# Kernel tuning notes

Hardware: AMD Instinct MI355X
Metric: run time of the kernel (lower is better)

## Reference

```python
import jax, jax.numpy as jnp
import numpy as np

GROUPS = 32
EPS = 1e-5
NHEAD = 8


def group_norm(x, gamma, beta):
    # x: [B, C, T]
    B, C, T = x.shape
    xg = x.reshape(B, GROUPS, C // GROUPS, T)
    mean = xg.mean(axis=(2, 3), keepdims=True)
    var = xg.var(axis=(2, 3), keepdims=True)
    xg = (xg - mean) * jax.lax.rsqrt(var + EPS)
    x = xg.reshape(B, C, T)
    return x * gamma[None, :, None] + beta[None, :, None]


def conv1x1(x, w, b):
    # x: [B, C_in, T], w: [C_out, C_in], b: [C_out]
    return jnp.einsum('oc,bct->bot', w, x) + b[None, :, None]


def setup_inputs() -> dict:
    key = jax.random.key(0)
    ks = jax.random.split(key, 4)
    B, C, T = 8, 512, 2048
    x = jax.random.normal(ks[0], (B, C, T), dtype=jnp.float32)
    w_qkv = jax.random.normal(ks[1], (3 * C, C), dtype=jnp.float32) * (1.0 / np.sqrt(C))
    b_qkv = jnp.zeros((3 * C,), dtype=jnp.float32)
    w_proj = jax.random.normal(ks[2], (C, C), dtype=jnp.float32) * (1.0 / np.sqrt(C))
    b_proj = jnp.zeros((C,), dtype=jnp.float32)
    return {
        'x': x,
        'gn1_gamma': jnp.ones((C,), jnp.float32), 'gn1_beta': jnp.zeros((C,), jnp.float32),
        'w_qkv': w_qkv, 'b_qkv': b_qkv,
        'gn2_gamma': jnp.ones((C,), jnp.float32), 'gn2_beta': jnp.zeros((C,), jnp.float32),
        'w_proj': w_proj, 'b_proj': b_proj,
    }


def qkv_attention(qkv):
    # qkv: [B, 3*H*ch, T] laid out as H blocks of (q ch, k ch, v ch)
    B, width, T = qkv.shape
    ch = width // (3 * NHEAD)
    qkv = qkv.reshape(B, NHEAD, 3 * ch, T)
    q, k, v = qkv[:, :, :ch], qkv[:, :, ch:2 * ch], qkv[:, :, 2 * ch:]
    scale = 1.0 / np.sqrt(np.sqrt(ch)).astype(np.float32)
    # scores: [B, H, T(q), T(k)]
    w = jnp.einsum('bhct,bhcs->bhts', q * scale, k * scale)
    w = jax.nn.softmax(w, axis=-1)  # max-subtract softmax, same math
    a = jnp.einsum('bhts,bhcs->bhct', w, v)
    return a.reshape(B, NHEAD * ch, T)


def reference(x, gn1_gamma, gn1_beta, w_qkv, b_qkv, gn2_gamma, gn2_beta, w_proj, b_proj):
    # x: [B, C, T]
    qkv = conv1x1(group_norm(x, gn1_gamma, gn1_beta), w_qkv, b_qkv)  # [B, 3C, T]
    h = qkv_attention(qkv)                                            # [B, C, T]
    h = conv1x1(group_norm(h, gn2_gamma, gn2_beta), w_proj, b_proj)   # [B, C, T]
    return x + h
```

## Files before the change

### kernel.cpp

```cpp
#include <hip/hip_runtime.h>

typedef unsigned short u16;
typedef unsigned int   u32;
typedef __attribute__((ext_vector_type(8))) short short8;
typedef __attribute__((ext_vector_type(4))) float floatx4;

__device__ inline u16 f2bf(float x) {
  union { float f; unsigned u; } v; v.f = x;
  unsigned r = v.u + 0x7FFFu + ((v.u >> 16) & 1u);
  return (u16)(r >> 16);
}
__device__ inline float bf2f(short s) {
  union { u32 u; float f; } v; v.u = ((u32)(u16)s) << 16; return v.f;
}
__device__ inline short8 ld8(const u16* p) {
  return *reinterpret_cast<const short8*>(p);
}
__device__ inline void async_ld16(const u16* g, u16* l) {
  unsigned loff = (unsigned)(unsigned long long)(void*)l;
  __builtin_amdgcn_global_load_lds(reinterpret_cast<const unsigned*>(g),
      reinterpret_cast<__attribute__((address_space(3))) unsigned*>(loff), 16, 0, 0);
}

__global__ __launch_bounds__(1024) void gncast(const float* __restrict__ x,
                                               const float* __restrict__ gamma,
                                               const float* __restrict__ beta,
                                               u16* __restrict__ xn,
                                               const float* __restrict__ wq,
                                               u16* __restrict__ wqb,
                                               const float* __restrict__ wp,
                                               u16* __restrict__ wpb) {
  __shared__ u16 tile[16 * 2048];
  float* stats = (float*)tile;
  const int tid = threadIdx.x;
  if (blockIdx.x >= 256) {
    int i = (blockIdx.x - 256) * 1024 + tid;
    const float* src; u16* dst; int j;
    if (i < 196608) { src = wq; dst = wqb; j = i; }
    else            { src = wp; dst = wpb; j = i - 196608; }
    float4 v = reinterpret_cast<const float4*>(src)[j];
    union { u16 u[4]; float2 f; } w;
    w.u[0] = f2bf(v.x); w.u[1] = f2bf(v.y); w.u[2] = f2bf(v.z); w.u[3] = f2bf(v.w);
    reinterpret_cast<float2*>(dst)[j] = w.f;
    return;
  }
  int b = blockIdx.x >> 5, g = blockIdx.x & 31;
  const float* base = x + ((long)b * 512 + g * 16) * 2048;
  float s = 0.f, ss = 0.f;
  for (int i = tid; i < 8192; i += 1024) {
    float4 v = reinterpret_cast<const float4*>(base)[i];
    s  += v.x + v.y + v.z + v.w;
    ss += v.x * v.x + v.y * v.y + v.z * v.z + v.w * v.w;
    int c = i >> 9, t4 = (i & 511) * 4;
    union { u16 u[4]; float2 f; } w;
    w.u[0] = f2bf(v.x); w.u[1] = f2bf(v.y); w.u[2] = f2bf(v.z); w.u[3] = f2bf(v.w);
    *reinterpret_cast<float2*>(&tile[c * 2048 + t4]) = w.f;
  }
  #pragma unroll
  for (int d = 1; d < 64; d <<= 1) { s += __shfl_xor(s, d); ss += __shfl_xor(ss, d); }
  __syncthreads();
  int wave = tid >> 6, lane = tid & 63;
  if (lane == 0) { stats[wave] = s; stats[wave + 16] = ss; }
  __syncthreads();
  s = 0.f; ss = 0.f;
  #pragma unroll
  for (int w = 0; w < 16; w++) { s += stats[w]; ss += stats[w + 16]; }
  float mean = s * (1.f / 32768.f);
  float var  = ss * (1.f / 32768.f) - mean * mean;
  float rstd = rsqrtf(var + 1e-5f);
  float ga[16], be[16];
  #pragma unroll
  for (int c = 0; c < 16; c++) {
    float gm = gamma[g * 16 + c];
    ga[c] = gm * rstd;
    be[c] = beta[g * 16 + c] - mean * rstd * gm;
  }
  u16* ob = xn + (long)b * 2048 * 512 + g * 16;
  #pragma unroll
  for (int tt = 0; tt < 2; tt++) {
    int t = tid * 2 + tt;
    union { u16 u[8]; float4 f; } w0, w1;
    #pragma unroll
    for (int c = 0; c < 16; c++) {
      float f;
      if (c == 0 && t < 64) f = base[t];
      else                  f = bf2f((short)tile[c * 2048 + t]);
      u16 o = f2bf(f * ga[c] + be[c]);
      if (c < 8) w0.u[c] = o; else w1.u[c - 8] = o;
    }
    u16* dst = ob + (long)t * 512;
    *reinterpret_cast<float4*>(dst)     = w0.f;
    *reinterpret_cast<float4*>(dst + 8) = w1.f;
  }
}

__global__ __launch_bounds__(1024) void gn_tc(const u16* __restrict__ a,
                                              const float* __restrict__ gamma,
                                              const float* __restrict__ beta,
                                              u16* __restrict__ hn) {
  int b = blockIdx.x >> 5, g = blockIdx.x & 31;
  const u16* base = a + (long)b * 2048 * 512 + g * 16;
  float s = 0.f, ss = 0.f;
  for (int t = threadIdx.x; t < 2048; t += 1024) {
    const u16* p = base + (long)t * 512;
    short8 v0 = ld8(p), v1 = ld8(p + 8);
    #pragma unroll
    for (int j = 0; j < 8; j++) {
      float f0 = bf2f(v0[j]), f1 = bf2f(v1[j]);
      s += f0 + f1; ss += f0 * f0 + f1 * f1;
    }
  }
  #pragma unroll
  for (int d = 1; d < 64; d <<= 1) { s += __shfl_xor(s, d); ss += __shfl_xor(ss, d); }
  __shared__ float red[32];
  int wave = threadIdx.x >> 6, lane = threadIdx.x & 63;
  if (lane == 0) { red[wave] = s; red[wave + 16] = ss; }
  __syncthreads();
  s = 0.f; ss = 0.f;
  #pragma unroll
  for (int w = 0; w < 16; w++) { s += red[w]; ss += red[w + 16]; }
  float mean = s * (1.f / 32768.f);
  float var  = ss * (1.f / 32768.f) - mean * mean;
  float rstd = rsqrtf(var + 1e-5f);
  float ga[16], be[16];
  #pragma unroll
  for (int c = 0; c < 16; c++) {
    float gm = gamma[g * 16 + c];
    ga[c] = gm * rstd;
    be[c] = beta[g * 16 + c] - mean * rstd * gm;
  }
  u16* ob = hn + (long)b * 2048 * 512 + g * 16;
  for (int t = threadIdx.x; t < 2048; t += 1024) {
    const u16* p = base + (long)t * 512;
    short8 v0 = ld8(p), v1 = ld8(p + 8);
    union { u16 u[8]; float4 f; } w0, w1;
    #pragma unroll
    for (int c = 0; c < 8; c++)  w0.u[c] = f2bf(bf2f(v0[c]) * ga[c] + be[c]);
    #pragma unroll
    for (int c = 0; c < 8; c++)  w1.u[c] = f2bf(bf2f(v1[c]) * ga[c + 8] + be[c + 8]);
    u16* dst = ob + (long)t * 512;
    *reinterpret_cast<float4*>(dst)     = w0.f;
    *reinterpret_cast<float4*>(dst + 8) = w1.f;
  }
}

template<int QKV>
__global__ __launch_bounds__(256) void gemm_tn(
    const u16* __restrict__ A, long abst,
    const u16* __restrict__ Bt, long bbst,
    const float* __restrict__ bias,
    const float* __restrict__ resid, long rbst,
    void* __restrict__ outp, long obst,
    u16* __restrict__ vtp, int K) {
  __shared__ __align__(16) u16 As[2][128 * 32];
  __shared__ __align__(16) u16 Bs[2][128 * 32];
  const int tid = threadIdx.x;
  const int m0 = blockIdx.y * 128, n0 = blockIdx.x * 128;
  const int N = gridDim.x * 128;
  const long bz = blockIdx.z;
  const u16* Ab = A + bz * abst + (long)m0 * K;
  const u16* Bb = Bt + bz * bbst + (long)n0 * K;
  const int lane = tid & 63, wave = tid >> 6;
  const int wm = (wave & 1) * 64, wn = (wave >> 1) * 64;
  const int l15 = lane & 15, quad = lane >> 4;
  const u16* ag[2]; const u16* bg[2];
  const int ldso = wave * 512;
  #pragma unroll
  for (int half = 0; half < 2; half++) {
    int r = half * 64 + (tid >> 2);
    ag[half] = Ab + (long)r * K + (tid & 3) * 8;
    bg[half] = Bb + (long)r * K + (tid & 3) * 8;
  }

  floatx4 acc[4][4];
  #pragma unroll
  for (int i = 0; i < 4; i++)
    #pragma unroll
    for (int j = 0; j < 4; j++) acc[i][j] = (floatx4){0.f, 0.f, 0.f, 0.f};

  #pragma unroll
  for (int half = 0; half < 2; half++) {
    async_ld16(ag[half], &As[0][half * 2048 + ldso]);
    async_ld16(bg[half], &Bs[0][half * 2048 + ldso]);
  }
  const int nk = K >> 5;
  for (int ki = 0; ki < nk; ki++) {
    __syncthreads();
    if (ki + 1 < nk) {
      int k1 = (ki + 1) << 5, bsel = (ki + 1) & 1;
      #pragma unroll
      for (int half = 0; half < 2; half++) {
        async_ld16(ag[half] + k1, &As[bsel][half * 2048 + ldso]);
        async_ld16(bg[half] + k1, &Bs[bsel][half * 2048 + ldso]);
      }
    }
    const u16* as = As[ki & 1]; const u16* bs = Bs[ki & 1];
    short8 af[4], bfr[4];
    #pragma unroll
    for (int i = 0; i < 4; i++) af[i]  = ld8(&as[(wm + i * 16 + l15) * 32 + quad * 8]);
    #pragma unroll
    for (int i = 0; i < 4; i++) bfr[i] = ld8(&bs[(wn + i * 16 + l15) * 32 + quad * 8]);
    #pragma unroll
    for (int mi = 0; mi < 4; mi++)
      #pragma unroll
      for (int ni = 0; ni < 4; ni++)
        acc[mi][ni] = __builtin_amdgcn_mfma_f32_16x16x32_bf16(af[mi], bfr[ni], acc[mi][ni], 0, 0, 0);
  }

  if (QKV) {
    u16* D  = (u16*)outp + bz * obst;
    u16* VT = vtp + bz * (8L * 64 * 2048);
    #pragma unroll
    for (int ni = 0; ni < 4; ni++) {
      int nb = n0 + wn + ni * 16;
      int region = (nb >> 6) % 3;
      int n = nb + l15;
      float bn = bias[n];
      if (region == 2) {
        int hh = n / 192, c = (n % 192) - 128;
        u16* vrow = VT + ((long)hh * 64 + c) * 2048 + m0 + wm;
        #pragma unroll
        for (int mi = 0; mi < 4; mi++) {
          union { u16 u[4]; float2 f; } pk;
          #pragma unroll
          for (int r = 0; r < 4; r++) pk.u[r] = f2bf(acc[mi][ni][r] + bn);
          *reinterpret_cast<float2*>(vrow + mi * 16 + quad * 4) = pk.f;
        }
      } else {
        float sc = (region == 0) ? 0.180336880f : 1.f;
        #pragma unroll
        for (int mi = 0; mi < 4; mi++)
          #pragma unroll
          for (int r = 0; r < 4; r++) {
            int m = m0 + wm + mi * 16 + quad * 4 + r;
            D[(long)m * 1536 + n] = f2bf((acc[mi][ni][r] + bn) * sc);
          }
      }
    }
  } else {
    float* D = (float*)outp + bz * obst;
    const float* R = resid + bz * rbst;
    #pragma unroll
    for (int mi = 0; mi < 4; mi++)
      #pragma unroll
      for (int r = 0; r < 4; r++) {
        int m = m0 + wm + mi * 16 + quad * 4 + r;
        float bm = bias[m];
        #pragma unroll
        for (int ni = 0; ni < 4; ni++) {
          int n = n0 + wn + ni * 16 + l15;
          long idx = (long)m * N + n;
          D[idx] = acc[mi][ni][r] + bm + R[idx];
        }
      }
  }
}

__global__ __launch_bounds__(512, 4) void attn(const u16* __restrict__ qkv,
                                               const u16* __restrict__ vt,
                                               u16* __restrict__ aout) {
  __shared__ __align__(16) u16 Ks[2][64 * 64];
  __shared__ __align__(16) u16 Vs[2][64 * 64];
  const int tid = threadIdx.x, lane = tid & 63, wave = tid >> 6;
  const int l15 = lane & 15, quad = lane >> 4;
  const int sw = l15 & 7;
  const int bh = blockIdx.x & 63;
  const int b = bh >> 3, h = bh & 7;
  const int t0 = (blockIdx.x >> 6) * 256;
  const u16* qbase = qkv + (long)b * 2048 * 1536 + h * 192;
  const u16* vbase = vt + (long)(b * 8 + h) * 64 * 2048;

  short8 qf[2][2];
  #pragma unroll
  for (int tqi = 0; tqi < 2; tqi++)
    #pragma unroll
    for (int ks = 0; ks < 2; ks++)
      qf[tqi][ks] = ld8(qbase + (long)(t0 + wave * 32 + tqi * 16 + l15) * 1536 + ks * 32 + quad * 8);

  short8 ones;
  #pragma unroll
  for (int j = 0; j < 8; j++) ones[j] = (short)0x3F80;

  const int prow = tid >> 3, pc = (tid & 7) ^ (prow & 7);
  const u16* kg = qbase + (long)prow * 1536 + 64 + pc * 8;
  const u16* vg = vbase + (long)prow * 2048 + pc * 8;
  const int ldso = wave * 512;
  async_ld16(kg, &Ks[0][ldso]);
  async_ld16(vg, &Vs[0][ldso]);

  floatx4 accO[4][2];
  floatx4 lacc[2];
  #pragma unroll
  for (int ci = 0; ci < 4; ci++)
    #pragma unroll
    for (int tqi = 0; tqi < 2; tqi++) accO[ci][tqi] = (floatx4){0.f, 0.f, 0.f, 0.f};
  #pragma unroll
  for (int tqi = 0; tqi < 2; tqi++) lacc[tqi] = (floatx4){0.f, 0.f, 0.f, 0.f};

  for (int it = 0; it < 32; it++) {
    const u16* kb = Ks[it & 1];
    const u16* vb = Vs[it & 1];
    __syncthreads();
    if (it < 31) {
      int s1 = (it + 1) * 64;
      async_ld16(kg + (long)s1 * 1536, &Ks[(it & 1) ^ 1][ldso]);
      async_ld16(vg + s1,              &Vs[(it & 1) ^ 1][ldso]);
    }

    floatx4 sacc[4][2];
    #pragma unroll
    for (int i = 0; i < 4; i++)
      #pragma unroll
      for (int j = 0; j < 2; j++) sacc[i][j] = (floatx4){0.f, 0.f, 0.f, 0.f};
    #pragma unroll
    for (int ks = 0; ks < 2; ks++) {
      short8 kf[4];
      #pragma unroll
      for (int tki = 0; tki < 4; tki++)
        kf[tki] = ld8(&kb[((tki * 16 + l15) << 6) + (((ks * 4 + quad) ^ sw) << 3)]);
      #pragma unroll
      for (int tki = 0; tki < 4; tki++)
        #pragma unroll
        for (int tqi = 0; tqi < 2; tqi++)
          sacc[tki][tqi] = __builtin_amdgcn_mfma_f32_16x16x32_bf16(kf[tki], qf[tqi][ks], sacc[tki][tqi], 0, 0, 0);
    }

    #pragma unroll
    for (int tki = 0; tki < 4; tki++)
      #pragma unroll
      for (int tqi = 0; tqi < 2; tqi++)
        #pragma unroll
        for (int r = 0; r < 4; r++)
          sacc[tki][tqi][r] = __builtin_amdgcn_exp2f(sacc[tki][tqi][r]);

    #pragma unroll
    for (int ks = 0; ks < 2; ks++) {
      short8 vf[4], pf[2];
      #pragma unroll
      for (int ci = 0; ci < 4; ci++)
        vf[ci] = ld8(&vb[((ci * 16 + l15) << 6) + (((ks * 4 + quad) ^ sw) << 3)]);
      #pragma unroll
      for (int tqi = 0; tqi < 2; tqi++) {
        u32 a0 = __builtin_amdgcn_perm(__float_as_uint(sacc[2 * ks][tqi][1]),
                                       __float_as_uint(sacc[2 * ks][tqi][0]), 0x07060302);
        u32 a1 = __builtin_amdgcn_perm(__float_as_uint(sacc[2 * ks][tqi][3]),
                                       __float_as_uint(sacc[2 * ks][tqi][2]), 0x07060302);
        u32 b0 = __builtin_amdgcn_perm(__float_as_uint(sacc[2 * ks + 1][tqi][1]),
                                       __float_as_uint(sacc[2 * ks + 1][tqi][0]), 0x07060302);
        u32 b1 = __builtin_amdgcn_perm(__float_as_uint(sacc[2 * ks + 1][tqi][3]),
                                       __float_as_uint(sacc[2 * ks + 1][tqi][2]), 0x07060302);
        auto u0 = __builtin_amdgcn_permlane32_swap(a0, b0, false, false);
        auto v0 = __builtin_amdgcn_permlane16_swap(u0[0], u0[1], false, false);
        auto u1 = __builtin_amdgcn_permlane32_swap(a1, b1, false, false);
        auto v1 = __builtin_amdgcn_permlane16_swap(u1[0], u1[1], false, false);
        union { u32 w[4]; short8 s8; } pw;
        pw.w[0] = v0[0]; pw.w[1] = v1[0]; pw.w[2] = v0[1]; pw.w[3] = v1[1];
        pf[tqi] = pw.s8;
      }
      #pragma unroll
      for (int tqi = 0; tqi < 2; tqi++)
        lacc[tqi] = __builtin_amdgcn_mfma_f32_16x16x32_bf16(ones, pf[tqi], lacc[tqi], 0, 0, 0);
      #pragma unroll
      for (int ci = 0; ci < 4; ci++)
        #pragma unroll
        for (int tqi = 0; tqi < 2; tqi++)
          accO[ci][tqi] = __builtin_amdgcn_mfma_f32_16x16x32_bf16(vf[ci], pf[tqi], accO[ci][tqi], 0, 0, 0);
    }
  }

  u16* ob = aout + ((long)b * 2048 + t0 + wave * 32) * 512 + h * 64;
  #pragma unroll
  for (int tqi = 0; tqi < 2; tqi++) {
    float invl = 1.f / lacc[tqi][0];
    #pragma unroll
    for (int ci = 0; ci < 4; ci++) {
      union { u16 u[4]; float2 f; } pk;
      #pragma unroll
      for (int r = 0; r < 4; r++) pk.u[r] = f2bf(accO[ci][tqi][r] * invl);
      *reinterpret_cast<float2*>(ob + (long)(tqi * 16 + l15) * 512 + ci * 16 + quad * 4) = pk.f;
    }
  }
}

extern "C" void kernel_launch(void* const* d_in, const int* in_sizes, int n_in,
                              void* d_out, int out_size, void* d_ws, size_t ws_size,
                              hipStream_t stream) {
  const float* x   = (const float*)d_in[0];
  const float* g1  = (const float*)d_in[1];
  const float* be1 = (const float*)d_in[2];
  const float* wq  = (const float*)d_in[3];
  const float* bq  = (const float*)d_in[4];
  const float* g2  = (const float*)d_in[5];
  const float* be2 = (const float*)d_in[6];
  const float* wp  = (const float*)d_in[7];
  const float* bp  = (const float*)d_in[8];

  char* ws = (char*)d_ws;
  u16*   xn   = (u16*)ws;
  u16*   a    = (u16*)ws;
  u16*   qkvb = (u16*)(ws + 33554432);
  u16*   hn   = (u16*)(ws + 83886080);
  u16*   vtb  = hn;
  u16*   wqb  = (u16*)(ws + 100663296);
  u16*   wpb  = (u16*)(ws + 102236160);

  gncast<<<512, 1024, 0, stream>>>(x, g1, be1, xn, wq, wqb, wp, wpb);
  gemm_tn<1><<<dim3(12, 16, 8), 256, 0, stream>>>(
      xn, (long)2048 * 512, wqb, 0, bq, nullptr, 0, qkvb, (long)2048 * 1536, vtb, 512);
  attn<<<512, 512, 0, stream>>>(qkvb, vtb, a);
  gn_tc<<<256, 1024, 0, stream>>>(a, g2, be2, hn);
  gemm_tn<0><<<dim3(16, 4, 8), 256, 0, stream>>>(
      wpb, 0, hn, (long)2048 * 512, bp, x, (long)512 * 2048, d_out, (long)512 * 2048, nullptr, 512);
}
```

Measured before the change: 263.2 us.

## Load K and V fragments directly from global memory in attention, dropping LDS staging

The attention kernel no longer stages K and V tiles through double-buffered shared memory with async global-to-LDS copies. Each wave now reads its MFMA fragments straight from global memory, and V fragments are issued before the exp step. This removes the block-wide barrier and the LDS round trip. In exchange, every wave fetches the same K/V data separately, and global latency is exposed without a software prefetch.

```diff
diff --git a/kernel.cpp b/kernel.cpp
--- a/kernel.cpp
+++ b/kernel.cpp
@@ -259,11 +259,8 @@
 __global__ __launch_bounds__(512, 4) void attn(const u16* __restrict__ qkv,
                                                const u16* __restrict__ vt,
                                                u16* __restrict__ aout) {
-  __shared__ __align__(16) u16 Ks[2][64 * 64];
-  __shared__ __align__(16) u16 Vs[2][64 * 64];
   const int tid = threadIdx.x, lane = tid & 63, wave = tid >> 6;
   const int l15 = lane & 15, quad = lane >> 4;
-  const int sw = l15 & 7;
   const int bh = blockIdx.x & 63;
   const int b = bh >> 3, h = bh & 7;
   const int t0 = (blockIdx.x >> 6) * 256;
@@ -281,12 +278,8 @@
   #pragma unroll
   for (int j = 0; j < 8; j++) ones[j] = (short)0x3F80;
 
-  const int prow = tid >> 3, pc = (tid & 7) ^ (prow & 7);
-  const u16* kg = qbase + (long)prow * 1536 + 64 + pc * 8;
-  const u16* vg = vbase + (long)prow * 2048 + pc * 8;
-  const int ldso = wave * 512;
-  async_ld16(kg, &Ks[0][ldso]);
-  async_ld16(vg, &Vs[0][ldso]);
+  const u16* kfp = qbase + (long)l15 * 1536 + 64 + quad * 8;
+  const u16* vfp = vbase + (long)l15 * 2048 + quad * 8;
 
   floatx4 accO[4][2];
   floatx4 lacc[2];
@@ -298,14 +291,8 @@
   for (int tqi = 0; tqi < 2; tqi++) lacc[tqi] = (floatx4){0.f, 0.f, 0.f, 0.f};
 
   for (int it = 0; it < 32; it++) {
-    const u16* kb = Ks[it & 1];
-    const u16* vb = Vs[it & 1];
-    __syncthreads();
-    if (it < 31) {
-      int s1 = (it + 1) * 64;
-      async_ld16(kg + (long)s1 * 1536, &Ks[(it & 1) ^ 1][ldso]);
-      async_ld16(vg + s1,              &Vs[(it & 1) ^ 1][ldso]);
-    }
+    const u16* kit = kfp + (long)(it * 64) * 1536;
+    const u16* vit = vfp + it * 64;
 
     floatx4 sacc[4][2];
     #pragma unroll
@@ -317,7 +304,7 @@
       short8 kf[4];
       #pragma unroll
       for (int tki = 0; tki < 4; tki++)
-        kf[tki] = ld8(&kb[((tki * 16 + l15) << 6) + (((ks * 4 + quad) ^ sw) << 3)]);
+        kf[tki] = ld8(kit + (long)(tki * 16) * 1536 + ks * 32);
       #pragma unroll
       for (int tki = 0; tki < 4; tki++)
         #pragma unroll
@@ -325,6 +312,13 @@
           sacc[tki][tqi] = __builtin_amdgcn_mfma_f32_16x16x32_bf16(kf[tki], qf[tqi][ks], sacc[tki][tqi], 0, 0, 0);
     }
 
+    short8 vf[4][2];
+    #pragma unroll
+    for (int ks = 0; ks < 2; ks++)
+      #pragma unroll
+      for (int ci = 0; ci < 4; ci++)
+        vf[ci][ks] = ld8(vit + (long)(ci * 16) * 2048 + ks * 32);
+
     #pragma unroll
     for (int tki = 0; tki < 4; tki++)
       #pragma unroll
@@ -335,10 +329,7 @@
 
     #pragma unroll
     for (int ks = 0; ks < 2; ks++) {
-      short8 vf[4], pf[2];
-      #pragma unroll
-      for (int ci = 0; ci < 4; ci++)
-        vf[ci] = ld8(&vb[((ci * 16 + l15) << 6) + (((ks * 4 + quad) ^ sw) << 3)]);
+      short8 pf[2];
       #pragma unroll
       for (int tqi = 0; tqi < 2; tqi++) {
         u32 a0 = __builtin_amdgcn_perm(__float_as_uint(sacc[2 * ks][tqi][1]),
@@ -364,7 +355,7 @@
       for (int ci = 0; ci < 4; ci++)
         #pragma unroll
         for (int tqi = 0; tqi < 2; tqi++)
-          accO[ci][tqi] = __builtin_amdgcn_mfma_f32_16x16x32_bf16(vf[ci], pf[tqi], accO[ci][tqi], 0, 0, 0);
+          accO[ci][tqi] = __builtin_amdgcn_mfma_f32_16x16x32_bf16(vf[ci][ks], pf[tqi], accO[ci][tqi], 0, 0, 0);
     }
   }
 
```

Result: slower. 427.8 us (+62.6%).

## Software-pipeline attention loop: overlap next QK MFMA with previous PV MFMA

Applied to the files above, without the earlier changes.

Restructures the attention inner loop so each iteration computes QK scores for the current key block while doing the PV accumulation for the previous block's probabilities, adding a third V shared-memory buffer and a prologue and epilogue. The goal is to hide the exp/permute latency between the score MFMAs and the PV MFMAs by interleaving independent matrix work. The cost is more live registers (pf and the vfr fragments held across stages), which could reduce occupancy under the 512-thread, 4-block launch bounds, plus extra LDS for the third buffer.

```diff
diff --git a/kernel.cpp b/kernel.cpp
--- a/kernel.cpp
+++ b/kernel.cpp
@@ -260,7 +260,7 @@
                                                const u16* __restrict__ vt,
                                                u16* __restrict__ aout) {
   __shared__ __align__(16) u16 Ks[2][64 * 64];
-  __shared__ __align__(16) u16 Vs[2][64 * 64];
+  __shared__ __align__(16) u16 Vs[3][64 * 64];
   const int tid = threadIdx.x, lane = tid & 63, wave = tid >> 6;
   const int l15 = lane & 15, quad = lane >> 4;
   const int sw = l15 & 7;
@@ -285,8 +285,12 @@
   const u16* kg = qbase + (long)prow * 1536 + 64 + pc * 8;
   const u16* vg = vbase + (long)prow * 2048 + pc * 8;
   const int ldso = wave * 512;
+
+  u16* vprev = &Vs[2][0];
+  u16* vcur  = &Vs[0][0];
+  u16* vnext = &Vs[1][0];
   async_ld16(kg, &Ks[0][ldso]);
-  async_ld16(vg, &Vs[0][ldso]);
+  async_ld16(vg, vcur + ldso);
 
   floatx4 accO[4][2];
   floatx4 lacc[2];
@@ -297,17 +301,9 @@
   #pragma unroll
   for (int tqi = 0; tqi < 2; tqi++) lacc[tqi] = (floatx4){0.f, 0.f, 0.f, 0.f};
 
-  for (int it = 0; it < 32; it++) {
-    const u16* kb = Ks[it & 1];
-    const u16* vb = Vs[it & 1];
-    __syncthreads();
-    if (it < 31) {
-      int s1 = (it + 1) * 64;
-      async_ld16(kg + (long)s1 * 1536, &Ks[(it & 1) ^ 1][ldso]);
-      async_ld16(vg + s1,              &Vs[(it & 1) ^ 1][ldso]);
-    }
-
-    floatx4 sacc[4][2];
+  short8 pf[2][2];
+
+  auto SBLOCK = [&](const u16* kb, floatx4 (&sacc)[4][2]) {
     #pragma unroll
     for (int i = 0; i < 4; i++)
       #pragma unroll
@@ -324,7 +320,23 @@
         for (int tqi = 0; tqi < 2; tqi++)
           sacc[tki][tqi] = __builtin_amdgcn_mfma_f32_16x16x32_bf16(kf[tki], qf[tqi][ks], sacc[tki][tqi], 0, 0, 0);
     }
-
+  };
+
+  auto PVBLOCK = [&](short8 (&vfr)[4][2]) {
+    #pragma unroll
+    for (int ks = 0; ks < 2; ks++) {
+      #pragma unroll
+      for (int tqi = 0; tqi < 2; tqi++)
+        lacc[tqi] = __builtin_amdgcn_mfma_f32_16x16x32_bf16(ones, pf[ks][tqi], lacc[tqi], 0, 0, 0);
+      #pragma unroll
+      for (int ci = 0; ci < 4; ci++)
+        #pragma unroll
+        for (int tqi = 0; tqi < 2; tqi++)
+          accO[ci][tqi] = __builtin_amdgcn_mfma_f32_16x16x32_bf16(vfr[ci][ks], pf[ks][tqi], accO[ci][tqi], 0, 0, 0);
+    }
+  };
+
+  auto EPBLOCK = [&](floatx4 (&sacc)[4][2]) {
     #pragma unroll
     for (int tki = 0; tki < 4; tki++)
       #pragma unroll
@@ -332,13 +344,8 @@
         #pragma unroll
         for (int r = 0; r < 4; r++)
           sacc[tki][tqi][r] = __builtin_amdgcn_exp2f(sacc[tki][tqi][r]);
-
-    #pragma unroll
-    for (int ks = 0; ks < 2; ks++) {
-      short8 vf[4], pf[2];
-      #pragma unroll
-      for (int ci = 0; ci < 4; ci++)
-        vf[ci] = ld8(&vb[((ci * 16 + l15) << 6) + (((ks * 4 + quad) ^ sw) << 3)]);
+    #pragma unroll
+    for (int ks = 0; ks < 2; ks++)
       #pragma unroll
       for (int tqi = 0; tqi < 2; tqi++) {
         u32 a0 = __builtin_amdgcn_perm(__float_as_uint(sacc[2 * ks][tqi][1]),
@@ -355,17 +362,61 @@
         auto v1 = __builtin_amdgcn_permlane16_swap(u1[0], u1[1], false, false);
         union { u32 w[4]; short8 s8; } pw;
         pw.w[0] = v0[0]; pw.w[1] = v1[0]; pw.w[2] = v0[1]; pw.w[3] = v1[1];
-        pf[tqi] = pw.s8;
+        pf[ks][tqi] = pw.s8;
       }
-      #pragma unroll
-      for (int tqi = 0; tqi < 2; tqi++)
-        lacc[tqi] = __builtin_amdgcn_mfma_f32_16x16x32_bf16(ones, pf[tqi], lacc[tqi], 0, 0, 0);
+  };
+
+  {
+    __syncthreads();
+    async_ld16(kg + (long)64 * 1536, &Ks[1][ldso]);
+    async_ld16(vg + 64, vnext + ldso);
+    floatx4 sacc[4][2];
+    SBLOCK(&Ks[0][0], sacc);
+    EPBLOCK(sacc);
+    u16* t = vprev; vprev = vcur; vcur = vnext; vnext = t;
+  }
+
+  for (int it = 1; it < 31; it++) {
+    __syncthreads();
+    int s1 = (it + 1) * 64;
+    async_ld16(kg + (long)s1 * 1536, &Ks[(it & 1) ^ 1][ldso]);
+    async_ld16(vg + s1, vnext + ldso);
+    short8 vfr[4][2];
+    #pragma unroll
+    for (int ks = 0; ks < 2; ks++)
       #pragma unroll
       for (int ci = 0; ci < 4; ci++)
-        #pragma unroll
-        for (int tqi = 0; tqi < 2; tqi++)
-          accO[ci][tqi] = __builtin_amdgcn_mfma_f32_16x16x32_bf16(vf[ci], pf[tqi], accO[ci][tqi], 0, 0, 0);
-    }
+        vfr[ci][ks] = ld8(&vprev[((ci * 16 + l15) << 6) + (((ks * 4 + quad) ^ sw) << 3)]);
+    floatx4 sacc[4][2];
+    SBLOCK(&Ks[it & 1][0], sacc);
+    PVBLOCK(vfr);
+    EPBLOCK(sacc);
+    u16* t = vprev; vprev = vcur; vcur = vnext; vnext = t;
+  }
+
+  {
+    __syncthreads();
+    short8 vfr[4][2];
+    #pragma unroll
+    for (int ks = 0; ks < 2; ks++)
+      #pragma unroll
+      for (int ci = 0; ci < 4; ci++)
+        vfr[ci][ks] = ld8(&vprev[((ci * 16 + l15) << 6) + (((ks * 4 + quad) ^ sw) << 3)]);
+    floatx4 sacc[4][2];
+    SBLOCK(&Ks[1][0], sacc);
+    PVBLOCK(vfr);
+    EPBLOCK(sacc);
+    u16* t = vprev; vprev = vcur; vcur = vnext; vnext = t;
+  }
+
+  {
+    short8 vfr[4][2];
+    #pragma unroll
+    for (int ks = 0; ks < 2; ks++)
+      #pragma unroll
+      for (int ci = 0; ci < 4; ci++)
+        vfr[ci][ks] = ld8(&vprev[((ci * 16 + l15) << 6) + (((ks * 4 + quad) ^ sw) << 3)]);
+    PVBLOCK(vfr);
   }
 
   u16* ob = aout + ((long)b * 2048 + t0 + wave * 32) * 512 + h * 64;
```

New measurement: 268.2 us. Within noise of the previous version (+1.9%).
